# Optimization experiments

Measured on AMD Instinct MI355X. Metric: run time of the kernel, lower is better.

Reference implementation:

```python
import jax, jax.numpy as jnp
import numpy as np

T, H, E, K = 16384, 4096, 8, 2
AUX_COEF = 0.01


def setup_inputs() -> dict:
    key = jax.random.key(0)
    k1, k2 = jax.random.split(key)
    hidden_states = jax.random.normal(k1, (T, H), dtype=jnp.float32)
    # nn.Linear weight, shape [n_experts, hidden_size], scaled like default init
    gate_w = jax.random.normal(k2, (E, H), dtype=jnp.float32) * (1.0 / np.sqrt(H))
    return {"hidden_states": hidden_states, "gate_w": gate_w}


def reference(hidden_states, gate_w):
    # router_logits: [T, E]
    router_logits = jnp.einsum("th,eh->te", hidden_states, gate_w)

    # softmax routing (routing_type == 'softmax')
    probs = jax.nn.softmax(router_logits, axis=-1)          # [T, E]
    routing_weights, selected_experts = jax.lax.top_k(probs, K)  # [T, K]
    routing_weights = routing_weights / jnp.sum(routing_weights, axis=-1, keepdims=True)

    # Switch-style load-balance aux loss (training mode):
    # f_i = fraction of tokens whose TOP-1 expert is i (scatter of selected_experts[:, :1])
    top1 = selected_experts[:, 0]                            # [T]
    f = jnp.mean(jax.nn.one_hot(top1, E, dtype=router_logits.dtype), axis=0)  # [E]
    P = jnp.mean(probs, axis=0)                              # [E]
    aux_loss = AUX_COEF * E * jnp.sum(f * P)

    return routing_weights, selected_experts, router_logits, aux_loss
```

## Files before the change

### kernel.cpp

```cpp
#include <hip/hip_runtime.h>
#include <math.h>


#define T_TOKENS 16384
#define H_DIM    4096
#define NEXP     8
#define H4       (H_DIM / 4)
#define ITERS    (H4 / 64)
#define TOK_PER_WAVE 4
#define WAVES_PER_BLOCK 4
#define TOK_PER_BLOCK (TOK_PER_WAVE * WAVES_PER_BLOCK)
#define NBLOCKS (T_TOKENS / TOK_PER_BLOCK)

#define OFF_RW  0
#define OFF_SE  32768
#define OFF_LG  65536
#define OFF_AUX 196608

typedef float vfloat4 __attribute__((ext_vector_type(4)));

#define RED_STEP(OFFSET, N)                                        \
  {                                                                \
    const bool hi = (lane & (OFFSET)) != 0;                        \
    _Pragma("unroll")                                              \
    for (int i = 0; i < (N); ++i) {                                \
      float send = hi ? r[i] : r[i + (N)];                         \
      float recv = __shfl_xor(send, (OFFSET), 64);                 \
      r[i] = (hi ? r[i + (N)] : r[i]) + recv;                      \
    }                                                              \
  }

#define LOAD_H(HV, KIDX)                                           \
  {                                                                \
    const int idx_ = lane + 64 * (KIDX);                           \
    _Pragma("unroll")                                              \
    for (int t = 0; t < TOK_PER_WAVE; ++t)                         \
      HV[t] = __builtin_nontemporal_load(                          \
          &h4p[(tokenBase + t) * H4 + idx_]);                      \
  }

#define GATE_AND_COMPUTE(HV, KIDX)                                 \
  {                                                                \
    const int idx_ = lane + 64 * (KIDX);                           \
    vfloat4 g[NEXP];                                               \
    _Pragma("unroll")                                              \
    for (int e = 0; e < NEXP; ++e) g[e] = g4p[e * H4 + idx_];      \
    _Pragma("unroll")                                              \
    for (int t = 0; t < TOK_PER_WAVE; ++t) {                       \
      _Pragma("unroll")                                            \
      for (int e = 0; e < NEXP; ++e) {                             \
        float a = r[t * NEXP + e];                                 \
        a = fmaf(HV[t].x, g[e].x, a);                              \
        a = fmaf(HV[t].y, g[e].y, a);                              \
        a = fmaf(HV[t].z, g[e].z, a);                              \
        a = fmaf(HV[t].w, g[e].w, a);                              \
        r[t * NEXP + e] = a;                                       \
      }                                                            \
    }                                                              \
  }

__global__ __launch_bounds__(256, 2)
void router_kernel(const float* __restrict__ hs, const float* __restrict__ gw,
                   float* __restrict__ out, float* __restrict__ ws) {
  __shared__ float smP[NEXP];
  __shared__ float smC[NEXP];
  if (threadIdx.x < NEXP) { smP[threadIdx.x] = 0.f; smC[threadIdx.x] = 0.f; }
  __syncthreads();

  const int lane = threadIdx.x & 63;
  const int wave = threadIdx.x >> 6;
  const int tokenBase = (blockIdx.x * WAVES_PER_BLOCK + wave) * TOK_PER_WAVE;

  const vfloat4* __restrict__ h4p = reinterpret_cast<const vfloat4*>(hs);
  const vfloat4* __restrict__ g4p = reinterpret_cast<const vfloat4*>(gw);

  float r[TOK_PER_WAVE * NEXP];
#pragma unroll
  for (int i = 0; i < TOK_PER_WAVE * NEXP; ++i) r[i] = 0.f;

  vfloat4 hvA[TOK_PER_WAVE], hvB[TOK_PER_WAVE];

  LOAD_H(hvA, 0)
  for (int k = 0; k < ITERS; k += 2) {
    LOAD_H(hvB, k + 1)
    GATE_AND_COMPUTE(hvA, k)
    if (k + 2 < ITERS) {
      LOAD_H(hvA, k + 2)
    }
    GATE_AND_COMPUTE(hvB, k + 1)
  }

  RED_STEP(16, 16)
  RED_STEP(8, 8)
  RED_STEP(4, 4)
  RED_STEP(2, 2)
  float red;
  {
    const bool hi = (lane & 1) != 0;
    float send = hi ? r[0] : r[1];
    float recv = __shfl_xor(send, 1, 64);
    red = (hi ? r[1] : r[0]) + recv;
  }
  red += __shfl_xor(red, 32, 64);

  if (lane < 32) out[OFF_LG + tokenBase * NEXP + lane] = red;

  float le[NEXP];
  const int groupBase = lane & 24;
#pragma unroll
  for (int e = 0; e < NEXP; ++e) le[e] = __shfl(red, groupBase + e, 64);

  if (lane < 32 && (lane & 7) == 0) {
    const int tok = tokenBase + (lane >> 3);
    int i1 = 0; float m1 = le[0];
#pragma unroll
    for (int e = 1; e < NEXP; ++e) {
      if (le[e] > m1) { m1 = le[e]; i1 = e; }
    }
    int i2 = (i1 == 0) ? 1 : 0; float m2 = le[i2];
#pragma unroll
    for (int e = 0; e < NEXP; ++e) {
      if (e != i1 && le[e] > m2) { m2 = le[e]; i2 = e; }
    }
    float p[NEXP];
    float psum = 0.f;
#pragma unroll
    for (int e = 0; e < NEXP; ++e) { p[e] = expf(le[e] - m1); psum += p[e]; }
    const float inv = 1.0f / psum;
#pragma unroll
    for (int e = 0; e < NEXP; ++e) atomicAdd(&smP[e], p[e] * inv);
    atomicAdd(&smC[i1], 1.0f);

    const float w1 = p[i1], w2 = p[i2];
    const float rs = 1.0f / (w1 + w2);
    out[OFF_RW + tok * 2 + 0] = w1 * rs;
    out[OFF_RW + tok * 2 + 1] = w2 * rs;
    out[OFF_SE + tok * 2 + 0] = (float)i1;
    out[OFF_SE + tok * 2 + 1] = (float)i2;
  }

  __syncthreads();
  if (threadIdx.x < 2 * NEXP) {
    const float v = (threadIdx.x < NEXP) ? smP[threadIdx.x]
                                         : smC[threadIdx.x - NEXP];
    ws[threadIdx.x * NBLOCKS + blockIdx.x] = v;
  }
}

__global__ __launch_bounds__(1024)
void aux_kernel(const float* __restrict__ ws, float* __restrict__ out) {
  __shared__ float sm[2 * NEXP];
  const int lane = threadIdx.x & 63;
  const int w = threadIdx.x >> 6;
  float s = 0.f;
#pragma unroll
  for (int i = 0; i < NBLOCKS / 64; ++i) s += ws[w * NBLOCKS + lane + 64 * i];
#pragma unroll
  for (int off = 32; off > 0; off >>= 1) s += __shfl_xor(s, off, 64);
  if (lane == 0) sm[w] = s;
  __syncthreads();
  if (threadIdx.x == 0) {
    const float invT = 1.0f / (float)T_TOKENS;
    float acc = 0.f;
#pragma unroll
    for (int e = 0; e < NEXP; ++e) {
      const float f = sm[NEXP + e] * invT;
      const float P = sm[e] * invT;
      acc += f * P;
    }
    out[OFF_AUX] = 0.01f * (float)NEXP * acc;
  }
}

extern "C" void kernel_launch(void* const* d_in, const int* in_sizes, int n_in,
                              void* d_out, int out_size, void* d_ws, size_t ws_size,
                              hipStream_t stream) {
  const float* hs = (const float*)d_in[0];
  const float* gw = (const float*)d_in[1];
  float* out = (float*)d_out;
  float* ws  = (float*)d_ws;

  router_kernel<<<NBLOCKS, 256, 0, stream>>>(hs, gw, out, ws);
  aux_kernel<<<1, 1024, 0, stream>>>(ws, out);
}
```

Baseline: 353.4 us.

## Halve tokens per wave and raise occupancy with a simpler single-buffered loop

Each wave now handles two tokens instead of four, and the launch bound asks for eight blocks per CU instead of two. The double-buffered prefetch loop is replaced by a plain loop that loads two hidden rows and processes the gate weights in two halves of four experts, which cuts live registers. The cross-lane reduction tree is rewritten to match the new 16-value accumulator layout. The intent is to hide memory latency with more resident waves rather than explicit prefetching, at the cost of reading the gate weights twice as often per token.

```diff
diff --git a/kernel.cpp b/kernel.cpp
--- a/kernel.cpp
+++ b/kernel.cpp
@@ -7,7 +7,7 @@
 #define NEXP     8
 #define H4       (H_DIM / 4)
 #define ITERS    (H4 / 64)
-#define TOK_PER_WAVE 4
+#define TOK_PER_WAVE 2
 #define WAVES_PER_BLOCK 4
 #define TOK_PER_BLOCK (TOK_PER_WAVE * WAVES_PER_BLOCK)
 #define NBLOCKS (T_TOKENS / TOK_PER_BLOCK)
@@ -30,36 +30,7 @@
     }                                                              \
   }
 
-#define LOAD_H(HV, KIDX)                                           \
-  {                                                                \
-    const int idx_ = lane + 64 * (KIDX);                           \
-    _Pragma("unroll")                                              \
-    for (int t = 0; t < TOK_PER_WAVE; ++t)                         \
-      HV[t] = __builtin_nontemporal_load(                          \
-          &h4p[(tokenBase + t) * H4 + idx_]);                      \
-  }
-
-#define GATE_AND_COMPUTE(HV, KIDX)                                 \
-  {                                                                \
-    const int idx_ = lane + 64 * (KIDX);                           \
-    vfloat4 g[NEXP];                                               \
-    _Pragma("unroll")                                              \
-    for (int e = 0; e < NEXP; ++e) g[e] = g4p[e * H4 + idx_];      \
-    _Pragma("unroll")                                              \
-    for (int t = 0; t < TOK_PER_WAVE; ++t) {                       \
-      _Pragma("unroll")                                            \
-      for (int e = 0; e < NEXP; ++e) {                             \
-        float a = r[t * NEXP + e];                                 \
-        a = fmaf(HV[t].x, g[e].x, a);                              \
-        a = fmaf(HV[t].y, g[e].y, a);                              \
-        a = fmaf(HV[t].z, g[e].z, a);                              \
-        a = fmaf(HV[t].w, g[e].w, a);                              \
-        r[t * NEXP + e] = a;                                       \
-      }                                                            \
-    }                                                              \
-  }
-
-__global__ __launch_bounds__(256, 2)
+__global__ __launch_bounds__(256, 8)
 void router_kernel(const float* __restrict__ hs, const float* __restrict__ gw,
                    float* __restrict__ out, float* __restrict__ ws) {
   __shared__ float smP[NEXP];
@@ -78,40 +49,51 @@
 #pragma unroll
   for (int i = 0; i < TOK_PER_WAVE * NEXP; ++i) r[i] = 0.f;
 
-  vfloat4 hvA[TOK_PER_WAVE], hvB[TOK_PER_WAVE];
-
-  LOAD_H(hvA, 0)
-  for (int k = 0; k < ITERS; k += 2) {
-    LOAD_H(hvB, k + 1)
-    GATE_AND_COMPUTE(hvA, k)
-    if (k + 2 < ITERS) {
-      LOAD_H(hvA, k + 2)
+  for (int k = 0; k < ITERS; ++k) {
+    const int idx = lane + 64 * k;
+    vfloat4 hv0 = __builtin_nontemporal_load(&h4p[(tokenBase + 0) * H4 + idx]);
+    vfloat4 hv1 = __builtin_nontemporal_load(&h4p[(tokenBase + 1) * H4 + idx]);
+#pragma unroll
+    for (int half = 0; half < 2; ++half) {
+      vfloat4 g[4];
+#pragma unroll
+      for (int e = 0; e < 4; ++e) g[e] = g4p[(half * 4 + e) * H4 + idx];
+#pragma unroll
+      for (int e = 0; e < 4; ++e) {
+        const int ei = half * 4 + e;
+        float a0 = r[0 * NEXP + ei];
+        float a1 = r[1 * NEXP + ei];
+        a0 = fmaf(hv0.x, g[e].x, a0); a1 = fmaf(hv1.x, g[e].x, a1);
+        a0 = fmaf(hv0.y, g[e].y, a0); a1 = fmaf(hv1.y, g[e].y, a1);
+        a0 = fmaf(hv0.z, g[e].z, a0); a1 = fmaf(hv1.z, g[e].z, a1);
+        a0 = fmaf(hv0.w, g[e].w, a0); a1 = fmaf(hv1.w, g[e].w, a1);
+        r[0 * NEXP + ei] = a0;
+        r[1 * NEXP + ei] = a1;
+      }
     }
-    GATE_AND_COMPUTE(hvB, k + 1)
   }
 
-  RED_STEP(16, 16)
-  RED_STEP(8, 8)
-  RED_STEP(4, 4)
-  RED_STEP(2, 2)
+  RED_STEP(32, 8)
+  RED_STEP(16, 4)
+  RED_STEP(8, 2)
   float red;
   {
-    const bool hi = (lane & 1) != 0;
+    const bool hi = (lane & 4) != 0;
     float send = hi ? r[0] : r[1];
-    float recv = __shfl_xor(send, 1, 64);
+    float recv = __shfl_xor(send, 4, 64);
     red = (hi ? r[1] : r[0]) + recv;
   }
-  red += __shfl_xor(red, 32, 64);
+  red += __shfl_xor(red, 2, 64);
+  red += __shfl_xor(red, 1, 64);
 
-  if (lane < 32) out[OFF_LG + tokenBase * NEXP + lane] = red;
+  if ((lane & 3) == 0) out[OFF_LG + tokenBase * NEXP + (lane >> 2)] = red;
 
   float le[NEXP];
-  const int groupBase = lane & 24;
 #pragma unroll
-  for (int e = 0; e < NEXP; ++e) le[e] = __shfl(red, groupBase + e, 64);
+  for (int e = 0; e < NEXP; ++e) le[e] = __shfl(red, (lane & 32) + (e << 2), 64);
 
-  if (lane < 32 && (lane & 7) == 0) {
-    const int tok = tokenBase + (lane >> 3);
+  if ((lane & 31) == 0) {
+    const int tok = tokenBase + (lane >> 5);
     int i1 = 0; float m1 = le[0];
 #pragma unroll
     for (int e = 1; e < NEXP; ++e) {
```

After: 363.1 us. 2.8% more time.
